# Kernel optimization log

Measured on AMD Instinct MI355X. Metric: run time of the kernel, lower is better.

The kernel has to match this reference:

```python
import jax, jax.numpy as jnp
import numpy as np

B, S, D = 1, 2048, 2048        # batch, max_seq_len, hidden_dim_attention
G, HPG = 4, 8                   # n_head_groups, n_heads_per_group
H = G * HPG                     # 32 total heads
DK = D // G                     # 512, KV projection width
HD = D // H                     # 64, head dim
EPS = 1e-6


def _embed_position(x, pm):
    # x: [B, S, d]; pm: [2, 1, S, D] -> uses pm[i][:, :, :d]
    d = x.shape[-1]
    _x = jnp.concatenate([-x[:, :, d // 2:], x[:, :, :d // 2]], axis=-1)
    # Faithful to source: BOTH terms use the rotated _x (source quirk).
    return _x * pm[0][:, :, :d] + _x * pm[1][:, :, :d]


def setup_inputs() -> dict:
    key = jax.random.key(0)
    k0, k1, k2, k3, k4, k5 = jax.random.split(key, 6)
    sc = 1.0 / np.sqrt(D).astype(np.float32)
    x = jax.random.normal(k0, (B, S, D), jnp.float32)
    position_matrix = jax.random.uniform(k1, (2, 1, S, D), jnp.float32)
    Wq = jax.random.normal(k2, (D, D), jnp.float32) * sc
    Wk = jax.random.normal(k3, (DK, D), jnp.float32) * sc
    Wv = jax.random.normal(k4, (DK, D), jnp.float32) * sc
    Wo = jax.random.normal(k5, (D, D), jnp.float32) * sc
    return {"x": x, "position_matrix": position_matrix,
            "Wq": Wq, "Wk": Wk, "Wv": Wv, "Wo": Wo}


def reference(x, position_matrix, Wq, Wk, Wv, Wo):
    xq = x @ Wq.T                                  # [B,S,D]
    xk = x @ Wk.T                                  # [B,S,DK]
    xv = x @ Wv.T                                  # [B,S,DK]
    xq = _embed_position(xq, position_matrix)
    xk = _embed_position(xk, position_matrix)
    # GQA expansion: replicate the DK-wide KV across G groups, split into heads.
    xk4 = jnp.broadcast_to(xk[:, :, None, :], (B, S, G, DK)).reshape(B, S, H, HD).transpose(0, 2, 1, 3)
    xv4 = jnp.broadcast_to(xv[:, :, None, :], (B, S, G, DK)).reshape(B, S, H, HD).transpose(0, 2, 1, 3)
    xq4 = xq.reshape(B, S, H, HD).transpose(0, 2, 1, 3)   # [B,H,S,HD]
    score = jnp.einsum('bhsd,bhtd->bhst', xq4, xk4) / (np.sqrt(DK) + EPS)
    # Source adds a tiny positive value (1e-10) above the diagonal, not -inf.
    mask = jnp.triu(jnp.full((S, S), 1e-10, jnp.float32), 1)
    score = score + mask
    e = jnp.exp(score.astype(jnp.float32))
    scores = (e / (jnp.sum(e, axis=-1, keepdims=True) + 1.0)).astype(xq4.dtype)
    out = jnp.einsum('bhst,bhtd->bhsd', scores, xv4)      # [B,H,S,HD]
    out = out.transpose(0, 2, 1, 3).reshape(B, S, D)
    return out @ Wo.T
```

## Files before the change

### kernel.cpp

```cpp
#include <hip/hip_runtime.h>
#include <cmath>

typedef unsigned short u16;
typedef unsigned int u32;
typedef __bf16 bf16x8 __attribute__((ext_vector_type(8)));
typedef __bf16 bf16x4 __attribute__((ext_vector_type(4)));
typedef float f32x4 __attribute__((ext_vector_type(4)));

#define S_LEN 2048
#define D_MODEL 2048
#define DK_ 512
#define PM1_OFF 4194304
#define CEXP 0.06375872f

__device__ __forceinline__ u16 f2b(float f) {
  u32 u = __float_as_uint(f);
  return (u16)((u + 0x7fffu + ((u >> 16) & 1u)) >> 16);
}

__device__ __forceinline__ void gload_lds16(const void* gp, void* lp) {
  __builtin_amdgcn_global_load_lds(
      (const __attribute__((address_space(1))) void*)gp,
      (__attribute__((address_space(3))) void*)lp, 16, 0, 0);
}

__device__ __forceinline__ void vmcnt0_barrier() {
  asm volatile("s_waitcnt vmcnt(0)" ::: "memory");
  __builtin_amdgcn_s_barrier();
}

__global__ __launch_bounds__(256) void cast_all_kernel(
    const float* __restrict__ x, const float* __restrict__ wq,
    const float* __restrict__ wk, const float* __restrict__ wv,
    const float* __restrict__ wo,
    u16* __restrict__ xb, u16* __restrict__ wqb, u16* __restrict__ wkb,
    u16* __restrict__ wvb, u16* __restrict__ wob)
{
  long i4 = (long)blockIdx.x * 256 + threadIdx.x;
  const float* src; u16* dst; long off;
  if (i4 < 1048576)       { src = x;  dst = xb;  off = i4; }
  else if (i4 < 2097152)  { src = wq; dst = wqb; off = i4 - 1048576; }
  else if (i4 < 2359296)  { src = wk; dst = wkb; off = i4 - 2097152; }
  else if (i4 < 2621440)  { src = wv; dst = wvb; off = i4 - 2359296; }
  else                    { src = wo; dst = wob; off = i4 - 2621440; }
  float4 v = *(const float4*)(src + off * 4);
  ushort4 o;
  o.x = f2b(v.x); o.y = f2b(v.y); o.z = f2b(v.z); o.w = f2b(v.w);
  *(ushort4*)(dst + off * 4) = o;
}

template<int EPI>
__global__ __launch_bounds__(256) void gemm_bt(
    const u16* __restrict__ A, const u16* __restrict__ B,
    void* __restrict__ C0, void* __restrict__ C1, void* __restrict__ C2,
    int M, int N, int K, const float* __restrict__ pm)
{
  __shared__ u16 As[2][64 * 64];
  __shared__ u16 Bs[2][128 * 64];
  const int tid = threadIdx.x;
  const int lane = tid & 63, w = tid >> 6;
  const int wr = w >> 1, wc = w & 1;
  const int l15 = lane & 15, l4 = lane >> 4;

  const int nwg = gridDim.x * gridDim.y;
  const int orig = blockIdx.y * gridDim.x + blockIdx.x;
  const int lin2 = (orig & 7) * (nwg >> 3) + (orig >> 3);
  const int m0 = (lin2 & 31) * 64;
  const int n0 = (lin2 >> 5) * 128;

  const int srow = tid >> 3;
  const int scol = ((tid & 7) ^ (srow & 7)) << 3;
  const int swz = (l15 & 7) << 3;
  const int ldsoff = (tid >> 6) << 10;
  const u16* gA = A + (size_t)(m0 + srow) * K + scol;
  const u16* gB = B + (size_t)(n0 + srow) * K + scol;

  const f32x4 z4 = {0.f, 0.f, 0.f, 0.f};
  f32x4 acc[2][4];
#pragma unroll
  for (int i = 0; i < 2; ++i)
#pragma unroll
    for (int j = 0; j < 4; ++j) acc[i][j] = z4;

  {
    char* la = (char*)As[0] + ldsoff;
    char* lb = (char*)Bs[0] + ldsoff;
#pragma unroll
    for (int i = 0; i < 2; ++i) gload_lds16(gA + (size_t)(i * 32) * K, la + i * 4096);
#pragma unroll
    for (int i = 0; i < 4; ++i) gload_lds16(gB + (size_t)(i * 32) * K, lb + i * 4096);
  }
  vmcnt0_barrier();

  const int NT = K >> 6;
  int cur = 0;
  for (int t = 0; t < NT; ++t) {
    if (t + 1 < NT) {
      const int kt = (t + 1) << 6;
      char* la = (char*)As[cur ^ 1] + ldsoff;
      char* lb = (char*)Bs[cur ^ 1] + ldsoff;
#pragma unroll
      for (int i = 0; i < 2; ++i) gload_lds16(gA + (size_t)(i * 32) * K + kt, la + i * 4096);
#pragma unroll
      for (int i = 0; i < 4; ++i) gload_lds16(gB + (size_t)(i * 32) * K + kt, lb + i * 4096);
    }
    const u16* as = As[cur];
    const u16* bs = Bs[cur];
#pragma unroll
    for (int ks = 0; ks < 2; ++ks) {
      bf16x8 a[2], b[4];
#pragma unroll
      for (int mt = 0; mt < 2; ++mt)
        a[mt] = *(const bf16x8*)(&as[(wr * 32 + mt * 16 + l15) * 64 + ((ks * 32 + l4 * 8) ^ swz)]);
#pragma unroll
      for (int nt = 0; nt < 4; ++nt)
        b[nt] = *(const bf16x8*)(&bs[(wc * 64 + nt * 16 + l15) * 64 + ((ks * 32 + l4 * 8) ^ swz)]);
#pragma unroll
      for (int mt = 0; mt < 2; ++mt)
#pragma unroll
        for (int nt = 0; nt < 4; ++nt)
          acc[mt][nt] = __builtin_amdgcn_mfma_f32_16x16x32_bf16(a[mt], b[nt], acc[mt][nt], 0, 0, 0);
    }
    vmcnt0_barrier();
    cur ^= 1;
  }

#pragma unroll
  for (int mt = 0; mt < 2; ++mt)
#pragma unroll
    for (int nt = 0; nt < 4; ++nt) {
      const int mb = m0 + wr * 32 + mt * 16 + l4 * 4;
      const int n = n0 + wc * 64 + nt * 16 + l15;
      if (EPI == 2) {
#pragma unroll
        for (int j = 0; j < 4; ++j)
          ((float*)C0)[(size_t)(mb + j) * N + n] = acc[mt][nt][j];
      } else if (n >= 2560) {
        const int c = n - 2560;
        ushort4 q;
        q.x = f2b(acc[mt][nt][0]); q.y = f2b(acc[mt][nt][1]);
        q.z = f2b(acc[mt][nt][2]); q.w = f2b(acc[mt][nt][3]);
        *(ushort4*)((u16*)C2 + (size_t)c * S_LEN + mb) = q;
      } else if (n < 2048) {
        const int jj = (n < 1024) ? (n + 1024) : (n - 1024);
#pragma unroll
        for (int j = 0; j < 4; ++j) {
          const int m = mb + j;
          const float sv = (n < 1024) ? acc[mt][nt][j] : -acc[mt][nt][j];
          const float p = pm[(size_t)m * D_MODEL + jj] +
                          pm[PM1_OFF + (size_t)m * D_MODEL + jj];
          ((u16*)C0)[(size_t)m * D_MODEL + jj] = f2b(sv * p * CEXP);
        }
      } else {
        const int nn = n - 2048;
        const int jj = (nn < 256) ? (nn + 256) : (nn - 256);
#pragma unroll
        for (int j = 0; j < 4; ++j) {
          const int m = mb + j;
          const float sv = (nn < 256) ? acc[mt][nt][j] : -acc[mt][nt][j];
          const float p = pm[(size_t)m * D_MODEL + jj] +
                          pm[PM1_OFF + (size_t)m * D_MODEL + jj];
          ((u16*)C1)[(size_t)m * DK_ + jj] = f2b(sv * p);
        }
      }
    }
}

__global__ __launch_bounds__(256) void attn_kernel(
    const u16* __restrict__ Q, const u16* __restrict__ Kx,
    const u16* __restrict__ Vt, u16* __restrict__ O)
{
  __shared__ u16 Ks[2][64 * 64];
  __shared__ u16 Vs[2][64 * 64];
  __shared__ u16 Es[4 * 16 * 64];

  const int tid = threadIdx.x;
  const int lane = tid & 63, w = tid >> 6;
  const int l15 = lane & 15, l4 = lane >> 4;

  const int orig = blockIdx.y * 32 + blockIdx.x;
  const int lin2 = (orig & 7) * 128 + (orig >> 3);
  const int h = lin2 >> 5;
  const int q0 = (lin2 & 31) * 64 + w * 16;
  const int hk = (h & 7) * 64;

  bf16x8 bq[2];
#pragma unroll
  for (int ks = 0; ks < 2; ++ks)
    bq[ks] = *(const bf16x8*)(Q + (size_t)(q0 + l15) * D_MODEL + h * 64 + ks * 32 + l4 * 8);

  bf16x8 b1;
#pragma unroll
  for (int i = 0; i < 8; ++i) b1[i] = (__bf16)1.0f;

  const f32x4 z4 = {0.f, 0.f, 0.f, 0.f};
  f32x4 o[4], dsum = z4;
#pragma unroll
  for (int nt = 0; nt < 4; ++nt) o[nt] = z4;

  u16* Ew = Es + w * (16 * 64);
  const int swz = (l15 & 7) << 3;
  const int srow = tid >> 3;
  const int scol = ((tid & 7) ^ (srow & 7)) << 3;
  const int ldsoff = w << 10;
  const u16* gK = Kx + (size_t)srow * DK_ + hk + scol;
  const u16* gV = Vt + (size_t)(hk + srow) * S_LEN + scol;

  {
    char* lK = (char*)Ks[0] + ldsoff;
    char* lV = (char*)Vs[0] + ldsoff;
    gload_lds16(gK,                        lK);
    gload_lds16(gK + (size_t)32 * DK_,     lK + 4096);
    gload_lds16(gV,                        lV);
    gload_lds16(gV + (size_t)32 * S_LEN,   lV + 4096);
  }
  vmcnt0_barrier();

  int cur = 0;
  for (int t0 = 0; t0 < S_LEN; t0 += 64) {
    if (t0 + 64 < S_LEN) {
      char* lK = (char*)Ks[cur ^ 1] + ldsoff;
      char* lV = (char*)Vs[cur ^ 1] + ldsoff;
      gload_lds16(gK + (size_t)(t0 + 64) * DK_,       lK);
      gload_lds16(gK + (size_t)(t0 + 96) * DK_,       lK + 4096);
      gload_lds16(gV + t0 + 64,                       lV);
      gload_lds16(gV + t0 + 64 + (size_t)32 * S_LEN,  lV + 4096);
    }
    const u16* ks_ = Ks[cur];
    const u16* vs_ = Vs[cur];

    f32x4 sT[4];
#pragma unroll
    for (int tf = 0; tf < 4; ++tf) sT[tf] = z4;
#pragma unroll
    for (int ks = 0; ks < 2; ++ks) {
      bf16x8 ak[4];
#pragma unroll
      for (int tf = 0; tf < 4; ++tf)
        ak[tf] = *(const bf16x8*)(&ks_[(tf * 16 + l15) * 64 + ((ks * 32 + l4 * 8) ^ swz)]);
      __builtin_amdgcn_s_setprio(1);
#pragma unroll
      for (int tf = 0; tf < 4; ++tf)
        sT[tf] = __builtin_amdgcn_mfma_f32_16x16x32_bf16(ak[tf], bq[ks], sT[tf], 0, 0, 0);
      __builtin_amdgcn_s_setprio(0);
    }

#pragma unroll
    for (int tf = 0; tf < 4; ++tf) {
      const float e0 = __builtin_amdgcn_exp2f(sT[tf][0]);
      const float e1 = __builtin_amdgcn_exp2f(sT[tf][1]);
      const float e2 = __builtin_amdgcn_exp2f(sT[tf][2]);
      const float e3 = __builtin_amdgcn_exp2f(sT[tf][3]);
      bf16x4 pk = {(__bf16)e0, (__bf16)e1, (__bf16)e2, (__bf16)e3};
      *(bf16x4*)(&Ew[l15 * 64 + ((tf * 16 + l4 * 4) ^ swz)]) = pk;
    }

#pragma unroll
    for (int ks = 0; ks < 2; ++ks) {
      const bf16x8 ae = *(const bf16x8*)(&Ew[l15 * 64 + ((ks * 32 + l4 * 8) ^ swz)]);
      bf16x8 bv[4];
#pragma unroll
      for (int nt = 0; nt < 4; ++nt)
        bv[nt] = *(const bf16x8*)(&vs_[(nt * 16 + l15) * 64 + ((ks * 32 + l4 * 8) ^ swz)]);
      __builtin_amdgcn_s_setprio(1);
#pragma unroll
      for (int nt = 0; nt < 4; ++nt)
        o[nt] = __builtin_amdgcn_mfma_f32_16x16x32_bf16(ae, bv[nt], o[nt], 0, 0, 0);
      dsum = __builtin_amdgcn_mfma_f32_16x16x32_bf16(ae, b1, dsum, 0, 0, 0);
      __builtin_amdgcn_s_setprio(0);
    }

    vmcnt0_barrier();
    cur ^= 1;
  }

  float dn[4];
#pragma unroll
  for (int j = 0; j < 4; ++j) dn[j] = dsum[j] + 1.0f;
#pragma unroll
  for (int nt = 0; nt < 4; ++nt)
#pragma unroll
    for (int j = 0; j < 4; ++j) {
      O[(size_t)(q0 + l4 * 4 + j) * D_MODEL + h * 64 + nt * 16 + l15] =
          f2b(o[nt][j] / dn[j]);
    }
}

extern "C" void kernel_launch(void* const* d_in, const int* in_sizes, int n_in,
                              void* d_out, int out_size, void* d_ws, size_t ws_size,
                              hipStream_t stream) {
  const float* x  = (const float*)d_in[0];
  const float* pm = (const float*)d_in[1];
  const float* Wq = (const float*)d_in[2];
  const float* Wk = (const float*)d_in[3];
  const float* Wv = (const float*)d_in[4];
  const float* Wo = (const float*)d_in[5];
  float* outp = (float*)d_out;
  char* ws = (char*)d_ws;

  const size_t MB = 1024 * 1024;
  u16* xb   = (u16*)(ws + 0 * MB);
  u16* wqb  = (u16*)(ws + 8 * MB);
  u16* wkb  = (u16*)(ws + 16 * MB);
  u16* wvb  = (u16*)(ws + 18 * MB);
  u16* wob  = (u16*)(ws + 20 * MB);
  u16* qro  = (u16*)(ws + 28 * MB);
  u16* kro  = (u16*)(ws + 36 * MB);
  u16* xvt  = (u16*)(ws + 40 * MB);
  u16* attn = (u16*)(ws + 42 * MB);
  const u16* wqkv = wqb;

  cast_all_kernel<<<14336, 256, 0, stream>>>(x, Wq, Wk, Wv, Wo, xb, wqb, wkb, wvb, wob);
  gemm_bt<1><<<dim3(24, 32), 256, 0, stream>>>(xb, wqkv, (void*)qro, (void*)kro,
                                               (void*)xvt, 2048, 3072, 2048, pm);
  attn_kernel<<<dim3(32, 32), 256, 0, stream>>>(qro, kro, xvt, attn);
  gemm_bt<2><<<dim3(16, 32), 256, 0, stream>>>(attn, wob, (void*)outp, nullptr,
                                               nullptr, 2048, 2048, 2048, nullptr);
}
```

Baseline: 140.7 us.

## Process two 16-row query groups per wave to reuse K/V tiles

Each wave in the attention kernel now handles 32 query rows (two 16-row groups) instead of 16, so each block covers 128 queries and the grid is halved. Every K/V tile loaded into shared memory and every K/V fragment read from it now feeds twice as many MFMAs, which cuts global and LDS traffic per unit of work. The cost is more registers for the extra accumulators and a larger per-wave E buffer, plus 512 blocks instead of 1024, which may lower occupancy and load balance across CUs.

Measured after the change: 134.7 us. -4.2%, faster.

```diff
diff --git a/kernel.cpp b/kernel.cpp
--- a/kernel.cpp
+++ b/kernel.cpp
@@ -172,33 +172,41 @@
 {
   __shared__ u16 Ks[2][64 * 64];
   __shared__ u16 Vs[2][64 * 64];
-  __shared__ u16 Es[4 * 16 * 64];
+  __shared__ u16 Es[4 * 32 * 64];
 
   const int tid = threadIdx.x;
   const int lane = tid & 63, w = tid >> 6;
   const int l15 = lane & 15, l4 = lane >> 4;
 
-  const int orig = blockIdx.y * 32 + blockIdx.x;
-  const int lin2 = (orig & 7) * 128 + (orig >> 3);
-  const int h = lin2 >> 5;
-  const int q0 = (lin2 & 31) * 64 + w * 16;
+  const int orig = blockIdx.y * 16 + blockIdx.x;
+  const int lin2 = (orig & 7) * 64 + (orig >> 3);
+  const int h = lin2 >> 4;
+  const int qb = lin2 & 15;
+  const int q0 = qb * 128 + w * 32;
   const int hk = (h & 7) * 64;
 
-  bf16x8 bq[2];
-#pragma unroll
-  for (int ks = 0; ks < 2; ++ks)
-    bq[ks] = *(const bf16x8*)(Q + (size_t)(q0 + l15) * D_MODEL + h * 64 + ks * 32 + l4 * 8);
+  bf16x8 bq[2][2];
+#pragma unroll
+  for (int g = 0; g < 2; ++g)
+#pragma unroll
+    for (int ks = 0; ks < 2; ++ks)
+      bq[g][ks] = *(const bf16x8*)(Q + (size_t)(q0 + g * 16 + l15) * D_MODEL
+                                     + h * 64 + ks * 32 + l4 * 8);
 
   bf16x8 b1;
 #pragma unroll
   for (int i = 0; i < 8; ++i) b1[i] = (__bf16)1.0f;
 
   const f32x4 z4 = {0.f, 0.f, 0.f, 0.f};
-  f32x4 o[4], dsum = z4;
-#pragma unroll
-  for (int nt = 0; nt < 4; ++nt) o[nt] = z4;
-
-  u16* Ew = Es + w * (16 * 64);
+  f32x4 o[2][4], dsum[2];
+#pragma unroll
+  for (int g = 0; g < 2; ++g) {
+    dsum[g] = z4;
+#pragma unroll
+    for (int nt = 0; nt < 4; ++nt) o[g][nt] = z4;
+  }
+
+  u16* Ew = Es + w * (32 * 64);
   const int swz = (l15 & 7) << 3;
   const int srow = tid >> 3;
   const int scol = ((tid & 7) ^ (srow & 7)) << 3;
@@ -229,9 +237,11 @@
     const u16* ks_ = Ks[cur];
     const u16* vs_ = Vs[cur];
 
-    f32x4 sT[4];
-#pragma unroll
-    for (int tf = 0; tf < 4; ++tf) sT[tf] = z4;
+    f32x4 sT[2][4];
+#pragma unroll
+    for (int g = 0; g < 2; ++g)
+#pragma unroll
+      for (int tf = 0; tf < 4; ++tf) sT[g][tf] = z4;
 #pragma unroll
     for (int ks = 0; ks < 2; ++ks) {
       bf16x8 ak[4];
@@ -240,33 +250,42 @@
         ak[tf] = *(const bf16x8*)(&ks_[(tf * 16 + l15) * 64 + ((ks * 32 + l4 * 8) ^ swz)]);
       __builtin_amdgcn_s_setprio(1);
 #pragma unroll
-      for (int tf = 0; tf < 4; ++tf)
-        sT[tf] = __builtin_amdgcn_mfma_f32_16x16x32_bf16(ak[tf], bq[ks], sT[tf], 0, 0, 0);
+      for (int g = 0; g < 2; ++g)
+#pragma unroll
+        for (int tf = 0; tf < 4; ++tf)
+          sT[g][tf] = __builtin_amdgcn_mfma_f32_16x16x32_bf16(ak[tf], bq[g][ks], sT[g][tf], 0, 0, 0);
       __builtin_amdgcn_s_setprio(0);
     }
 
 #pragma unroll
-    for (int tf = 0; tf < 4; ++tf) {
-      const float e0 = __builtin_amdgcn_exp2f(sT[tf][0]);
-      const float e1 = __builtin_amdgcn_exp2f(sT[tf][1]);
-      const float e2 = __builtin_amdgcn_exp2f(sT[tf][2]);
-      const float e3 = __builtin_amdgcn_exp2f(sT[tf][3]);
-      bf16x4 pk = {(__bf16)e0, (__bf16)e1, (__bf16)e2, (__bf16)e3};
-      *(bf16x4*)(&Ew[l15 * 64 + ((tf * 16 + l4 * 4) ^ swz)]) = pk;
-    }
+    for (int g = 0; g < 2; ++g)
+#pragma unroll
+      for (int tf = 0; tf < 4; ++tf) {
+        const float e0 = __builtin_amdgcn_exp2f(sT[g][tf][0]);
+        const float e1 = __builtin_amdgcn_exp2f(sT[g][tf][1]);
+        const float e2 = __builtin_amdgcn_exp2f(sT[g][tf][2]);
+        const float e3 = __builtin_amdgcn_exp2f(sT[g][tf][3]);
+        bf16x4 pk = {(__bf16)e0, (__bf16)e1, (__bf16)e2, (__bf16)e3};
+        *(bf16x4*)(&Ew[(g * 16 + l15) * 64 + ((tf * 16 + l4 * 4) ^ swz)]) = pk;
+      }
 
 #pragma unroll
     for (int ks = 0; ks < 2; ++ks) {
-      const bf16x8 ae = *(const bf16x8*)(&Ew[l15 * 64 + ((ks * 32 + l4 * 8) ^ swz)]);
-      bf16x8 bv[4];
+      bf16x8 ae[2], bv[4];
+#pragma unroll
+      for (int g = 0; g < 2; ++g)
+        ae[g] = *(const bf16x8*)(&Ew[(g * 16 + l15) * 64 + ((ks * 32 + l4 * 8) ^ swz)]);
 #pragma unroll
       for (int nt = 0; nt < 4; ++nt)
         bv[nt] = *(const bf16x8*)(&vs_[(nt * 16 + l15) * 64 + ((ks * 32 + l4 * 8) ^ swz)]);
       __builtin_amdgcn_s_setprio(1);
 #pragma unroll
-      for (int nt = 0; nt < 4; ++nt)
-        o[nt] = __builtin_amdgcn_mfma_f32_16x16x32_bf16(ae, bv[nt], o[nt], 0, 0, 0);
-      dsum = __builtin_amdgcn_mfma_f32_16x16x32_bf16(ae, b1, dsum, 0, 0, 0);
+      for (int g = 0; g < 2; ++g) {
+#pragma unroll
+        for (int nt = 0; nt < 4; ++nt)
+          o[g][nt] = __builtin_amdgcn_mfma_f32_16x16x32_bf16(ae[g], bv[nt], o[g][nt], 0, 0, 0);
+        dsum[g] = __builtin_amdgcn_mfma_f32_16x16x32_bf16(ae[g], b1, dsum[g], 0, 0, 0);
+      }
       __builtin_amdgcn_s_setprio(0);
     }
 
@@ -274,16 +293,19 @@
     cur ^= 1;
   }
 
-  float dn[4];
-#pragma unroll
-  for (int j = 0; j < 4; ++j) dn[j] = dsum[j] + 1.0f;
-#pragma unroll
-  for (int nt = 0; nt < 4; ++nt)
-#pragma unroll
-    for (int j = 0; j < 4; ++j) {
-      O[(size_t)(q0 + l4 * 4 + j) * D_MODEL + h * 64 + nt * 16 + l15] =
-          f2b(o[nt][j] / dn[j]);
-    }
+#pragma unroll
+  for (int g = 0; g < 2; ++g) {
+    float dn[4];
+#pragma unroll
+    for (int j = 0; j < 4; ++j) dn[j] = dsum[g][j] + 1.0f;
+#pragma unroll
+    for (int nt = 0; nt < 4; ++nt)
+#pragma unroll
+      for (int j = 0; j < 4; ++j) {
+        O[(size_t)(q0 + g * 16 + l4 * 4 + j) * D_MODEL + h * 64 + nt * 16 + l15] =
+            f2b(o[g][nt][j] / dn[j]);
+      }
+  }
 }
 
 extern "C" void kernel_launch(void* const* d_in, const int* in_sizes, int n_in,
@@ -313,7 +335,7 @@
   cast_all_kernel<<<14336, 256, 0, stream>>>(x, Wq, Wk, Wv, Wo, xb, wqb, wkb, wvb, wob);
   gemm_bt<1><<<dim3(24, 32), 256, 0, stream>>>(xb, wqkv, (void*)qro, (void*)kro,
                                                (void*)xvt, 2048, 3072, 2048, pm);
-  attn_kernel<<<dim3(32, 32), 256, 0, stream>>>(qro, kro, xvt, attn);
+  attn_kernel<<<dim3(16, 32), 256, 0, stream>>>(qro, kro, xvt, attn);
   gemm_bt<2><<<dim3(16, 32), 256, 0, stream>>>(attn, wob, (void*)outp, nullptr,
                                                nullptr, 2048, 2048, 2048, nullptr);
 }
```
